# Optimization experiments

Hardware: AMD Instinct MI355X
Metric: run time of the kernel (lower is better)

The kernel has to match this reference:

```python
import jax, jax.numpy as jnp
import numpy as np

H = 16          # num_attention_heads
HD = 64         # hidden_size_per_attention_head
EPS = 1e-12

def _layernorm(x, w, b):
    u = x.mean(-1, keepdims=True)
    s = ((x - u) ** 2).mean(-1, keepdims=True)
    return w * (x - u) / jnp.sqrt(s + EPS) + b

def _split_heads(x):
    b, s, d = x.shape
    return x.reshape(b, s, H, d // H).transpose(0, 2, 1, 3)  # [b,h,s,hd]

def _merge_heads(x):
    b, h, s, hd = x.shape
    return x.transpose(0, 2, 1, 3).reshape(b, s, h * hd)


def setup_inputs() -> dict:
    key = jax.random.key(0)
    ks = jax.random.split(key, 20)
    B, S, T, D, F = 4, 1024, 1024, 1024, 4096
    w = lambda k, shp: (jax.random.normal(k, shp, jnp.float32) * 0.02)
    return {
        "hidden_states": jax.random.normal(ks[0], (B, S, D), jnp.float32),
        "enc_hidden_states": jax.random.normal(ks[1], (B, T, D), jnp.float32),
        "enc_attn_mask": jnp.zeros((B, 1, 1, T), jnp.float32),
        "dec_attn_mask": jnp.tril(jnp.ones((S, S), jnp.float32)).reshape(1, 1, S, S),
        "ln1_w": jnp.ones((D,), jnp.float32), "ln1_b": jnp.zeros((D,), jnp.float32),
        "qkv_w": w(ks[2], (D, 3 * D)), "qkv_b": jnp.zeros((3 * D,), jnp.float32),
        "attn_o_w": w(ks[3], (D, D)), "attn_o_b": jnp.zeros((D,), jnp.float32),
        "ln2_w": jnp.ones((D,), jnp.float32), "ln2_b": jnp.zeros((D,), jnp.float32),
        "q_w": w(ks[4], (D, D)), "q_b": jnp.zeros((D,), jnp.float32),
        "kv_w": w(ks[5], (D, 2 * D)), "kv_b": jnp.zeros((2 * D,), jnp.float32),
        "ca_o_w": w(ks[6], (D, D)), "ca_o_b": jnp.zeros((D,), jnp.float32),
        "ln3_w": jnp.ones((D,), jnp.float32), "ln3_b": jnp.zeros((D,), jnp.float32),
        "ffn_in_w": w(ks[7], (D, F)), "ffn_in_b": jnp.zeros((F,), jnp.float32),
        "ffn_out_w": w(ks[8], (F, D)), "ffn_out_b": jnp.zeros((D,), jnp.float32),
    }


def reference(hidden_states, enc_hidden_states, enc_attn_mask, dec_attn_mask,
              ln1_w, ln1_b, qkv_w, qkv_b, attn_o_w, attn_o_b,
              ln2_w, ln2_b, q_w, q_b, kv_w, kv_b, ca_o_w, ca_o_b,
              ln3_w, ln3_b, ffn_in_w, ffn_in_b, ffn_out_w, ffn_out_b):
    scale = 1.0 / jnp.sqrt(jnp.float32(HD))
    # dropout layers are identity (eval mode)

    # ---- self-attention (ltor multiplicative mask formula) ----
    residual = hidden_states
    x = _layernorm(hidden_states, ln1_w, ln1_b)
    qkv = x @ qkv_w + qkv_b
    q, k, v = jnp.split(qkv, 3, axis=-1)
    q, k, v = _split_heads(q), _split_heads(k), _split_heads(v)
    scores = jnp.einsum('bhsd,bhtd->bhst', q, k) * scale
    scores = scores * dec_attn_mask - 10000.0 * (1.0 - dec_attn_mask)
    probs = jax.nn.softmax(scores, axis=-1)
    ctx = _merge_heads(jnp.einsum('bhst,bhtd->bhsd', probs, v))
    hidden_states = residual + (ctx @ attn_o_w + attn_o_b)

    # ---- cross-attention (additive enc mask) ----
    residual = hidden_states
    x = _layernorm(hidden_states, ln2_w, ln2_b)
    q = _split_heads(x @ q_w + q_b)
    kv = enc_hidden_states @ kv_w + kv_b
    k, v = jnp.split(kv, 2, axis=-1)
    k, v = _split_heads(k), _split_heads(v)
    scores = jnp.einsum('bhsd,bhtd->bhst', q, k) * scale + enc_attn_mask
    probs = jax.nn.softmax(scores, axis=-1)
    ctx = _merge_heads(jnp.einsum('bhst,bhtd->bhsd', probs, v))
    hidden_states = residual + (ctx @ ca_o_w + ca_o_b)

    # ---- FFN ----
    residual = hidden_states
    x = _layernorm(hidden_states, ln3_w, ln3_b)
    x = jax.nn.gelu(x @ ffn_in_w + ffn_in_b, approximate=False)
    x = x @ ffn_out_w + ffn_out_b
    return residual + x
```

## Files before the change

### kernel.cpp

```cpp
#include <hip/hip_runtime.h>
#include <cstdint>
#include <cstddef>

typedef unsigned short u16;
typedef __bf16 bf16x8 __attribute__((ext_vector_type(8)));
typedef float f32x4 __attribute__((ext_vector_type(4)));

__device__ __forceinline__ u16 f2bf(float f) {
  unsigned u = __float_as_uint(f);
  u += 0x7fffu + ((u >> 16) & 1u);
  return (u16)(u >> 16);
}

__device__ __forceinline__ float block_sum(float v, float* sbuf, int tid) {
#pragma unroll
  for (int off = 1; off < 64; off <<= 1) v += __shfl_xor(v, off, 64);
  if ((tid & 63) == 0) sbuf[tid >> 6] = v;
  __syncthreads();
  v = sbuf[0] + sbuf[1] + sbuf[2] + sbuf[3];
  __syncthreads();
  return v;
}

__device__ __forceinline__ void gld16(const void* g, void* l) {
  __builtin_amdgcn_global_load_lds((const __attribute__((address_space(1))) void*)g,
                                   (__attribute__((address_space(3))) void*)l,
                                   16, 0, 0);
}



#define BIG_PREAMBLE(BM, Kdim, KB)                                               \
  constexpr int NQA = (BM) / 64;                                                 \
  constexpr int IF  = (BM) / 32;                                                 \
  const int tid = threadIdx.x;                                                   \
  const int lane = tid & 63, wave = tid >> 6;                                    \
  const int l15 = lane & 15, g = (lane >> 4) & 3;                                \
  const int wr = (wave >> 2) * ((BM) / 2), wc = (wave & 3) * 64;                 \
  const int gx = gridDim.x;                                                      \
  const int nwg = gx * gridDim.y;                                                \
  const int id = blockIdx.y * gx + blockIdx.x;                                   \
  const int qq = nwg >> 3, rr = nwg & 7;                                         \
  const int xcd = id & 7, slot = id >> 3;                                        \
  const int sid = (xcd < rr ? xcd * (qq + 1) : rr * (qq + 1) + (xcd - rr) * qq) + slot; \
  const int bx = sid % gx, by = sid / gx;                                        \
  const int m0 = by * (BM), n0 = bx * 256;                                       \
  size_t aoff[NQA]; int adst[NQA];                                               \
  size_t boff[4];   int bdst[4];                                                 \
  _Pragma("unroll")                                                              \
  for (int q = 0; q < NQA; ++q) {                                                \
    const int c = tid + q * 512, row = c >> 3, ch = (c & 7) ^ (row & 7);         \
    aoff[q] = (size_t)(m0 + row) * (Kdim) + ch * 8 + (KB);                       \
    adst[q] = c * 8;                                                             \
  }                                                                              \
  _Pragma("unroll")                                                              \
  for (int q = 0; q < 4; ++q) {                                                  \
    const int c = tid + q * 512, row = c >> 3, ch = (c & 7) ^ (row & 7);         \
    boff[q] = (size_t)(n0 + row) * (Kdim) + ch * 8 + (KB);                       \
    bdst[q] = c * 8;                                                             \
  }

#define BIG_STAGE(BM, kk, buf)                                                   \
  {                                                                              \
    _Pragma("unroll")                                                            \
    for (int q = 0; q < NQA; ++q) gld16(A + aoff[q] + (kk), As + (buf) * ((BM) * 64) + adst[q]); \
    _Pragma("unroll")                                                            \
    for (int q = 0; q < 4; ++q)  gld16(B + boff[q] + (kk), Bs + (buf) * 16384 + bdst[q]); \
  }

#define BIG_COMPUTE(BM, buf)                                                     \
  {                                                                              \
    _Pragma("unroll")                                                            \
    for (int ks = 0; ks < 2; ++ks) {                                             \
      const int chR = (((ks * 4 + g) ^ (l15 & 7)) * 8);                          \
      bf16x8 af[IF], bg[4];                                                      \
      _Pragma("unroll")                                                          \
      for (int i = 0; i < IF; ++i)                                               \
        af[i] = *(const bf16x8*)(As + (buf) * ((BM) * 64) + (wr + i * 16 + l15) * 64 + chR); \
      _Pragma("unroll")                                                          \
      for (int j = 0; j < 4; ++j)                                                \
        bg[j] = *(const bf16x8*)(Bs + (buf) * 16384 + (wc + j * 16 + l15) * 64 + chR); \
      _Pragma("unroll")                                                          \
      for (int i = 0; i < IF; ++i)                                               \
        _Pragma("unroll")                                                        \
        for (int j = 0; j < 4; ++j)                                              \
          acc[i][j] = __builtin_amdgcn_mfma_f32_16x16x32_bf16(af[i], bg[j], acc[i][j], 0, 0, 0); \
    }                                                                            \
  }

#define BIG_WAIT_PREV(BM)                                                        \
  if constexpr ((BM) == 256)      asm volatile("s_waitcnt vmcnt(8)\ns_barrier" ::: "memory"); \
  else if constexpr ((BM) == 128) asm volatile("s_waitcnt vmcnt(6)\ns_barrier" ::: "memory"); \
  else                            asm volatile("s_waitcnt vmcnt(5)\ns_barrier" ::: "memory");

#define BIG_KLOOP(BM, NT)                                                        \
  f32x4 acc[IF][4] = {};                                                         \
  BIG_STAGE(BM, 0, 0)                                                            \
  int cur = 0;                                                                   \
  for (int t = 0; t < (NT) - 1; ++t) {                                           \
    BIG_STAGE(BM, (t + 1) * 64, cur ^ 1)                                         \
    BIG_WAIT_PREV(BM)                                                            \
    BIG_COMPUTE(BM, cur)                                                         \
    asm volatile("s_waitcnt lgkmcnt(0)\ns_barrier" ::: "memory");                \
    cur ^= 1;                                                                    \
  }                                                                              \
  asm volatile("s_waitcnt vmcnt(0)\ns_barrier" ::: "memory");                    \
  BIG_COMPUTE(BM, cur)

template<int BM, int MODE>
__global__ __launch_bounds__(512, 2) void gemm_big(
    const u16* __restrict__ A, const u16* __restrict__ B,
    const float* __restrict__ bias,
    u16* __restrict__ out0, u16* __restrict__ out1, u16* __restrict__ out2,
    int N, int K)
{
  __shared__ __align__(16) u16 As[2 * BM * 64];
  __shared__ __align__(16) u16 Bs[2 * 256 * 64];
  BIG_PREAMBLE(BM, K, 0)
  const int NT = K >> 6;
  BIG_KLOOP(BM, NT)

  if constexpr (MODE == 0) {
#pragma unroll
    for (int i = 0; i < IF; ++i) {
#pragma unroll
      for (int j = 0; j < 4; ++j) {
        const int col = n0 + wc + j * 16 + l15;
        const float bs = bias[col];
#pragma unroll
        for (int r = 0; r < 4; ++r) {
          const int gm = m0 + wr + i * 16 + g * 4 + r;
          float v = acc[i][j][r] + bs;
          v = 0.5f * v * (1.0f + erff(v * 0.70710678118654752f));
          out0[(size_t)gm * N + col] = f2bf(v);
        }
      }
    }
  } else {
#pragma unroll
    for (int i = 0; i < IF; ++i) {
#pragma unroll
      for (int j = 0; j < 4; ++j) {
        const int col = n0 + wc + j * 16 + l15;
        const int sec = (n0 + wc + j * 16) >> 10;
        const int tgt = (MODE == 1) ? sec : sec + 1;
        const float bs = bias[col];
#pragma unroll
        for (int r = 0; r < 4; ++r) {
          const int gm = m0 + wr + i * 16 + g * 4 + r;
          const float v = acc[i][j][r] + bs;
          const int cl = col & 1023, h = cl >> 6, d = cl & 63;
          const int z = (gm >> 10) * 16 + h, s = gm & 1023;
          if (tgt == 0)
            out0[((size_t)z * 1024 + s) * 64 + d] = f2bf(v * 0.125f);
          else if (tgt == 1)
            out1[((((size_t)z * 8 + (s >> 7)) * 8 + (d >> 3)) * 128 + (s & 127)) * 8 + (d & 7)] = f2bf(v);
          else
            out2[((size_t)z * 8 + (s >> 7)) * 8192 + (((s >> 3) & 15) * 64 + d) * 8 + (s & 7)] = f2bf(v);
        }
      }
    }
  }
}

template<int BM>
__global__ __launch_bounds__(512, 2) void gemm_part(
    const u16* __restrict__ A, const u16* __restrict__ B,
    float* __restrict__ part, int K, int Klen)
{
  __shared__ __align__(16) u16 As[2 * BM * 64];
  __shared__ __align__(16) u16 Bs[2 * 256 * 64];
  const int kb = blockIdx.z * Klen;
  float* outP = part + (size_t)blockIdx.z * (4096ULL * 1024);
  BIG_PREAMBLE(BM, K, kb)
  const int NT = Klen >> 6;
  BIG_KLOOP(BM, NT)

#pragma unroll
  for (int i = 0; i < IF; ++i)
#pragma unroll
    for (int j = 0; j < 4; ++j) {
      const int col = n0 + wc + j * 16 + l15;
#pragma unroll
      for (int r = 0; r < 4; ++r) {
        const int gm = m0 + wr + i * 16 + g * 4 + r;
        outP[(size_t)gm * 1024 + col] = acc[i][j][r];
      }
    }
}

__global__ __launch_bounds__(256, 2) void flash_attn(
    const u16* __restrict__ qh, const u16* __restrict__ kt, const u16* __restrict__ vt,
    const float* __restrict__ emask, u16* __restrict__ ctx, int causal)
{
  __shared__ __align__(16) u16 sK[8192];
  __shared__ __align__(16) u16 sV[8192];
  __shared__ __align__(16) u16 sP[128 * 72];

  const int tid = threadIdx.x, lane = tid & 63, wave = tid >> 6;
  const int l15 = lane & 15, g = (lane >> 4) & 3;
  const int id = blockIdx.y * 8 + blockIdx.x;
  const int xcd = id & 7, slot = id >> 3;
  const int z = xcd * 8 + (slot >> 3), b = z >> 4, h = z & 15;
  const int m0 = (slot & 7) * 128;
  const int r0 = wave * 32;

  bf16x8 qf[2][2];
  {
    const u16* qz = qh + ((size_t)z * 1024 + m0 + r0 + l15) * 64 + g * 8;
#pragma unroll
    for (int i2 = 0; i2 < 2; ++i2)
#pragma unroll
      for (int kc = 0; kc < 2; ++kc)
        qf[i2][kc] = *(const bf16x8*)(qz + (size_t)i2 * 16 * 64 + kc * 32);
  }

  float m_i[2][4], l_i[2][4];
#pragma unroll
  for (int i2 = 0; i2 < 2; ++i2)
#pragma unroll
    for (int r = 0; r < 4; ++r) { m_i[i2][r] = -1.0e30f; l_i[i2][r] = 0.0f; }

  f32x4 o[2][4] = {};
  const int tmax = causal ? m0 : 896;

  for (int t0 = 0; t0 <= tmax; t0 += 128) {
    const u16* ktile = kt + ((size_t)z * 8 + (t0 >> 7)) * 8192;
    const u16* vtile = vt + ((size_t)z * 8 + (t0 >> 7)) * 8192;
    __syncthreads();
#pragma unroll
    for (int i = 0; i < 4; ++i) {
      const int off = (wave * 4 + i) * 512 + lane * 8;
      gld16(ktile + off, sK + off);
      gld16(vtile + off, sV + off);
    }
    __syncthreads();

#pragma unroll
    for (int ci = 0; ci < 2; ++ci) {
      if (causal && t0 == m0 && ci * 64 > r0 + 31) continue;

      f32x4 sa[2][4] = {};
#pragma unroll
      for (int kc = 0; kc < 2; ++kc) {
        bf16x8 bg[4];
#pragma unroll
        for (int jn = 0; jn < 4; ++jn)
          bg[jn] = *(const bf16x8*)(sK + ((kc * 4 + g) * 128 + ci * 64 + jn * 16 + l15) * 8);
#pragma unroll
        for (int i2 = 0; i2 < 2; ++i2)
#pragma unroll
          for (int jn = 0; jn < 4; ++jn)
            sa[i2][jn] = __builtin_amdgcn_mfma_f32_16x16x32_bf16(qf[i2][kc], bg[jn], sa[i2][jn], 0, 0, 0);
      }

      if (causal) {
        if (t0 == m0 && ci * 64 + 63 > r0) {
#pragma unroll
          for (int i2 = 0; i2 < 2; ++i2)
#pragma unroll
            for (int jn = 0; jn < 4; ++jn) {
              const int col = ci * 64 + jn * 16 + l15;
#pragma unroll
              for (int r = 0; r < 4; ++r) {
                const int row = r0 + i2 * 16 + g * 4 + r;
                if (col > row) sa[i2][jn][r] = -3.0e38f;
              }
            }
        }
      } else {
#pragma unroll
        for (int jn = 0; jn < 4; ++jn) {
          const float mv = emask[(size_t)b * 1024 + t0 + ci * 64 + jn * 16 + l15];
#pragma unroll
          for (int i2 = 0; i2 < 2; ++i2)
#pragma unroll
            for (int r = 0; r < 4; ++r) sa[i2][jn][r] += mv;
        }
      }

      float alpha[2][4];
#pragma unroll
      for (int i2 = 0; i2 < 2; ++i2)
#pragma unroll
        for (int r = 0; r < 4; ++r) {
          const int rowl = r0 + i2 * 16 + g * 4 + r;
          float v = fmaxf(fmaxf(sa[i2][0][r], sa[i2][1][r]), fmaxf(sa[i2][2][r], sa[i2][3][r]));
          v = fmaxf(v, __shfl_xor(v, 1, 64));
          v = fmaxf(v, __shfl_xor(v, 2, 64));
          v = fmaxf(v, __shfl_xor(v, 4, 64));
          v = fmaxf(v, __shfl_xor(v, 8, 64));
          const float mo = m_i[i2][r];
          const float mn = fmaxf(mo, v);
          m_i[i2][r] = mn;
          alpha[i2][r] = __expf(mo - mn);
          float s = 0.0f;
#pragma unroll
          for (int jn = 0; jn < 4; ++jn) {
            const float p = __expf(sa[i2][jn][r] - mn);
            s += p;
            sP[rowl * 72 + jn * 16 + l15] = f2bf(p);
          }
          s += __shfl_xor(s, 1, 64);
          s += __shfl_xor(s, 2, 64);
          s += __shfl_xor(s, 4, 64);
          s += __shfl_xor(s, 8, 64);
          l_i[i2][r] = alpha[i2][r] * l_i[i2][r] + s;
        }

#pragma unroll
      for (int i2 = 0; i2 < 2; ++i2)
#pragma unroll
        for (int jn = 0; jn < 4; ++jn)
#pragma unroll
          for (int r = 0; r < 4; ++r)
            o[i2][jn][r] *= alpha[i2][r];

      asm volatile("s_waitcnt lgkmcnt(0)" ::: "memory");
#pragma unroll
      for (int kc2 = 0; kc2 < 2; ++kc2) {
        bf16x8 pa[2], vb[4];
#pragma unroll
        for (int i2 = 0; i2 < 2; ++i2)
          pa[i2] = *(const bf16x8*)(sP + (r0 + i2 * 16 + l15) * 72 + kc2 * 32 + g * 8);
#pragma unroll
        for (int jn = 0; jn < 4; ++jn)
          vb[jn] = *(const bf16x8*)(sV + ((ci * 8 + kc2 * 4 + g) * 64 + jn * 16 + l15) * 8);
#pragma unroll
        for (int i2 = 0; i2 < 2; ++i2)
#pragma unroll
          for (int jn = 0; jn < 4; ++jn)
            o[i2][jn] = __builtin_amdgcn_mfma_f32_16x16x32_bf16(pa[i2], vb[jn], o[i2][jn], 0, 0, 0);
      }
    }
  }

#pragma unroll
  for (int i2 = 0; i2 < 2; ++i2)
#pragma unroll
    for (int r = 0; r < 4; ++r) {
      const float inv = 1.0f / l_i[i2][r];
      const size_t base = ((size_t)(b * 1024 + m0 + r0 + i2 * 16 + g * 4 + r)) * 1024 + h * 64;
#pragma unroll
      for (int jn = 0; jn < 4; ++jn)
        ctx[base + jn * 16 + l15] = f2bf(o[i2][jn][r] * inv);
    }
}

struct PrepArgs {
  const float* w[7]; u16* wt[7]; int K[7]; int N[7]; int cum[7];
  const float* enc; u16* enc_bf;
  const float* hid; const float* ln1w; const float* ln1b; u16* xln;
};
__global__ __launch_bounds__(256) void prep_kernel(PrepArgs a) {
  __shared__ float t[32][33];
  __shared__ float sbuf[4];
  const int bb = blockIdx.x, tid = threadIdx.x;
  if (bb < 16384) {
    int wi = 0;
#pragma unroll
    for (int i = 0; i < 7; ++i) if (bb >= a.cum[i]) wi = i + 1; else break;
    const int base = wi ? a.cum[wi - 1] : 0;
    const int tileIdx = bb - base;
    const int Kd = a.K[wi], Nd = a.N[wi], nx = Nd >> 5;
    const int n0 = (tileIdx % nx) * 32, k0 = (tileIdx / nx) * 32;
    const float* w = a.w[wi]; u16* wt = a.wt[wi];
    const int tx = tid & 31, ty = tid >> 5;
#pragma unroll
    for (int r = ty; r < 32; r += 8) t[r][tx] = w[(size_t)(k0 + r) * Nd + n0 + tx];
    __syncthreads();
#pragma unroll
    for (int r = ty; r < 32; r += 8) wt[(size_t)(n0 + r) * Kd + k0 + tx] = f2bf(t[tx][r]);
  } else if (bb < 20480) {
    const size_t i = ((size_t)(bb - 16384) * 256 + tid) * 4;
    const float4 v = *(const float4*)(a.enc + i);
    ushort4 o; o.x = f2bf(v.x); o.y = f2bf(v.y); o.z = f2bf(v.z); o.w = f2bf(v.w);
    *(ushort4*)(a.enc_bf + i) = o;
  } else {
    const int row = bb - 20480;
    const float4 v = *(const float4*)(a.hid + (size_t)row * 1024 + tid * 4);
    float s = block_sum(v.x + v.y + v.z + v.w, sbuf, tid);
    const float u = s * (1.0f / 1024.0f);
    const float d0 = v.x - u, d1 = v.y - u, d2 = v.z - u, d3 = v.w - u;
    float sq = block_sum(d0 * d0 + d1 * d1 + d2 * d2 + d3 * d3, sbuf, tid);
    const float rstd = rsqrtf(sq * (1.0f / 1024.0f) + 1e-12f);
    const int c = tid * 4;
    ushort4 o;
    o.x = f2bf(a.ln1w[c + 0] * d0 * rstd + a.ln1b[c + 0]);
    o.y = f2bf(a.ln1w[c + 1] * d1 * rstd + a.ln1b[c + 1]);
    o.z = f2bf(a.ln1w[c + 2] * d2 * rstd + a.ln1b[c + 2]);
    o.w = f2bf(a.ln1w[c + 3] * d3 * rstd + a.ln1b[c + 3]);
    *(ushort4*)(a.xln + (size_t)row * 1024 + c) = o;
  }
}

__global__ __launch_bounds__(256) void ln_red1_kernel(
    const float* __restrict__ p0,
    const float* __restrict__ bias, const float* __restrict__ res,
    const float* __restrict__ w, const float* __restrict__ b,
    float* __restrict__ hOut, u16* __restrict__ xln)
{
  __shared__ float sbuf[4];
  const int row = blockIdx.x, tid = threadIdx.x;
  const size_t off = (size_t)row * 1024 + tid * 4;
  const int c = tid * 4;
  const float4 a0 = *(const float4*)(p0 + off);
  const float4 bs = *(const float4*)(bias + c);
  const float4 rs = *(const float4*)(res + off);
  float4 v;
  v.x = a0.x + bs.x + rs.x;
  v.y = a0.y + bs.y + rs.y;
  v.z = a0.z + bs.z + rs.z;
  v.w = a0.w + bs.w + rs.w;
  *(float4*)(hOut + off) = v;
  float s = block_sum(v.x + v.y + v.z + v.w, sbuf, tid);
  const float u = s * (1.0f / 1024.0f);
  const float d0 = v.x - u, d1 = v.y - u, d2 = v.z - u, d3 = v.w - u;
  float sq = block_sum(d0 * d0 + d1 * d1 + d2 * d2 + d3 * d3, sbuf, tid);
  const float rstd = rsqrtf(sq * (1.0f / 1024.0f) + 1e-12f);
  ushort4 o;
  o.x = f2bf(w[c + 0] * d0 * rstd + b[c + 0]);
  o.y = f2bf(w[c + 1] * d1 * rstd + b[c + 1]);
  o.z = f2bf(w[c + 2] * d2 * rstd + b[c + 2]);
  o.w = f2bf(w[c + 3] * d3 * rstd + b[c + 3]);
  *(ushort4*)(xln + off) = o;
}

__global__ __launch_bounds__(256) void reduce_q1_kernel(
    const float* __restrict__ p0,
    const float* __restrict__ bias, u16* __restrict__ qh)
{
  const int m = blockIdx.x, tid = threadIdx.x;
  const size_t off = (size_t)m * 1024 + tid * 4;
  const int n = tid * 4, h = n >> 6, d = n & 63;
  const int b = m >> 10, s = m & 1023;
  const float4 a0 = *(const float4*)(p0 + off);
  const float4 bs = *(const float4*)(bias + n);
  ushort4 o;
  o.x = f2bf((a0.x + bs.x) * 0.125f);
  o.y = f2bf((a0.y + bs.y) * 0.125f);
  o.z = f2bf((a0.z + bs.z) * 0.125f);
  o.w = f2bf((a0.w + bs.w) * 0.125f);
  *(ushort4*)(qh + ((size_t)((b * 16 + h) * 1024 + s)) * 64 + d) = o;
}

__global__ __launch_bounds__(256) void reduce_out_kernel(
    const float* __restrict__ p0, const float* __restrict__ p1,
    const float* __restrict__ bias, const float* __restrict__ res,
    float* __restrict__ out)
{
  const int m = blockIdx.x, tid = threadIdx.x;
  const size_t off = (size_t)m * 1024 + tid * 4;
  const int c = tid * 4;
  const float4 a0 = *(const float4*)(p0 + off);
  const float4 a1 = *(const float4*)(p1 + off);
  const float4 bs = *(const float4*)(bias + c);
  const float4 rs = *(const float4*)(res + off);
  float4 v;
  v.x = a0.x + a1.x + bs.x + rs.x;
  v.y = a0.y + a1.y + bs.y + rs.y;
  v.z = a0.z + a1.z + bs.z + rs.z;
  v.w = a0.w + a1.w + bs.w + rs.w;
  *(float4*)(out + off) = v;
}

constexpr size_t MB = 1024ULL * 1024;
constexpr size_t WT_QKV    = 0;
constexpr size_t WT_ATTN_O = 6 * MB;
constexpr size_t WT_Q      = 8 * MB;
constexpr size_t WT_KV     = 10 * MB;
constexpr size_t WT_CA_O   = 14 * MB;
constexpr size_t WT_FFN_IN = 16 * MB;
constexpr size_t WT_FFN_OUT= 24 * MB;
constexpr size_t ENC_BF    = 32 * MB;
constexpr size_t XLN       = 40 * MB;
constexpr size_t QH        = 48 * MB;
constexpr size_t KT        = 56 * MB;
constexpr size_t VT        = 64 * MB;
constexpr size_t CTX       = 72 * MB;
constexpr size_t HBUF      = 80 * MB;
constexpr size_t SP0       = 96 * MB;
constexpr size_t SP1       = 112 * MB;
constexpr size_t FFN_MID   = 128 * MB;

extern "C" void kernel_launch(void* const* d_in, const int* in_sizes, int n_in,
                              void* d_out, int out_size, void* d_ws, size_t ws_size,
                              hipStream_t stream) {
  const float* hidden   = (const float*)d_in[0];
  const float* enc      = (const float*)d_in[1];
  const float* encm     = (const float*)d_in[2];
  const float* ln1w = (const float*)d_in[4],  *ln1b = (const float*)d_in[5];
  const float* qkv_w = (const float*)d_in[6], *qkv_b = (const float*)d_in[7];
  const float* attn_o_w = (const float*)d_in[8], *attn_o_b = (const float*)d_in[9];
  const float* ln2w = (const float*)d_in[10], *ln2b = (const float*)d_in[11];
  const float* q_w = (const float*)d_in[12],  *q_b = (const float*)d_in[13];
  const float* kv_w = (const float*)d_in[14], *kv_b = (const float*)d_in[15];
  const float* ca_o_w = (const float*)d_in[16], *ca_o_b = (const float*)d_in[17];
  const float* ln3w = (const float*)d_in[18], *ln3b = (const float*)d_in[19];
  const float* ffn_in_w = (const float*)d_in[20], *ffn_in_b = (const float*)d_in[21];
  const float* ffn_out_w = (const float*)d_in[22], *ffn_out_b = (const float*)d_in[23];

  char* ws = (char*)d_ws;
  u16* wt_qkv    = (u16*)(ws + WT_QKV);
  u16* wt_attn_o = (u16*)(ws + WT_ATTN_O);
  u16* wt_q      = (u16*)(ws + WT_Q);
  u16* wt_kv     = (u16*)(ws + WT_KV);
  u16* wt_ca_o   = (u16*)(ws + WT_CA_O);
  u16* wt_ffn_in = (u16*)(ws + WT_FFN_IN);
  u16* wt_ffn_out= (u16*)(ws + WT_FFN_OUT);
  u16* enc_bf = (u16*)(ws + ENC_BF);
  u16* xln    = (u16*)(ws + XLN);
  u16* qh     = (u16*)(ws + QH);
  u16* kt     = (u16*)(ws + KT);
  u16* vt     = (u16*)(ws + VT);
  u16* ctx    = (u16*)(ws + CTX);
  float* hF   = (float*)(ws + HBUF);
  float* sp0  = (float*)(ws + SP0);
  float* sp1  = (float*)(ws + SP1);
  u16* ffn_mid = (u16*)(ws + FFN_MID);

  PrepArgs pa;
  pa.w[0] = qkv_w;    pa.wt[0] = wt_qkv;     pa.K[0] = 1024; pa.N[0] = 3072; pa.cum[0] = 3072;
  pa.w[1] = attn_o_w; pa.wt[1] = wt_attn_o;  pa.K[1] = 1024; pa.N[1] = 1024; pa.cum[1] = 4096;
  pa.w[2] = q_w;      pa.wt[2] = wt_q;       pa.K[2] = 1024; pa.N[2] = 1024; pa.cum[2] = 5120;
  pa.w[3] = kv_w;     pa.wt[3] = wt_kv;      pa.K[3] = 1024; pa.N[3] = 2048; pa.cum[3] = 7168;
  pa.w[4] = ca_o_w;   pa.wt[4] = wt_ca_o;    pa.K[4] = 1024; pa.N[4] = 1024; pa.cum[4] = 8192;
  pa.w[5] = ffn_in_w; pa.wt[5] = wt_ffn_in;  pa.K[5] = 1024; pa.N[5] = 4096; pa.cum[5] = 12288;
  pa.w[6] = ffn_out_w;pa.wt[6] = wt_ffn_out; pa.K[6] = 4096; pa.N[6] = 1024; pa.cum[6] = 16384;
  pa.enc = enc; pa.enc_bf = enc_bf;
  pa.hid = hidden; pa.ln1w = ln1w; pa.ln1b = ln1b; pa.xln = xln;
  prep_kernel<<<24576, 256, 0, stream>>>(pa);

  gemm_big<256, 1><<<dim3(12, 16), 512, 0, stream>>>(xln, wt_qkv, qkv_b, qh, kt, vt, 3072, 1024);
  flash_attn<<<dim3(8, 64), 256, 0, stream>>>(qh, kt, vt, nullptr, ctx, 1);
  gemm_part<64><<<dim3(4, 64, 1), 512, 0, stream>>>(ctx, wt_attn_o, sp0, 1024, 1024);
  ln_red1_kernel<<<4096, 256, 0, stream>>>(sp0, attn_o_b, hidden, ln2w, ln2b, hF, xln);

  gemm_part<64><<<dim3(4, 64, 1), 512, 0, stream>>>(xln, wt_q, sp0, 1024, 1024);
  reduce_q1_kernel<<<4096, 256, 0, stream>>>(sp0, q_b, qh);
  gemm_big<128, 3><<<dim3(8, 32), 512, 0, stream>>>(enc_bf, wt_kv, kv_b, nullptr, kt, vt, 2048, 1024);
  flash_attn<<<dim3(8, 64), 256, 0, stream>>>(qh, kt, vt, encm, ctx, 0);
  gemm_part<64><<<dim3(4, 64, 1), 512, 0, stream>>>(ctx, wt_ca_o, sp0, 1024, 1024);
  ln_red1_kernel<<<4096, 256, 0, stream>>>(sp0, ca_o_b, hF, ln3w, ln3b, hF, xln);

  gemm_big<256, 0><<<dim3(16, 16), 512, 0, stream>>>(xln, wt_ffn_in, ffn_in_b, ffn_mid, nullptr, nullptr, 4096, 1024);
  gemm_part<128><<<dim3(4, 32, 2), 512, 0, stream>>>(ffn_mid, wt_ffn_out, sp0, 4096, 2048);
  reduce_out_kernel<<<4096, 256, 0, stream>>>(sp0, sp1, ffn_out_b, hF, (float*)d_out);
}
```

Before: 555.4 us.

## Shrink flash-attention query tile to 64 rows and swizzle P buffer

The flash attention kernel now processes 64 query rows per block (16 per wave) instead of 128, doubling the grid and raising the occupancy hint from 2 to 4 blocks per SM. The P staging buffer becomes a compact 64x64 tile with an XOR swizzle in place of row padding, to avoid LDS bank conflicts. More, smaller blocks should balance the causal triangle better and hide latency, but each K/V tile is now loaded from global memory twice as often.

Result: no change. 558.2 us (+0.5%).

```diff
diff --git a/kernel.cpp b/kernel.cpp
--- a/kernel.cpp
+++ b/kernel.cpp
@@ -189,40 +189,38 @@
     }
 }
 
-__global__ __launch_bounds__(256, 2) void flash_attn(
+__global__ __launch_bounds__(256, 4) void flash_attn(
     const u16* __restrict__ qh, const u16* __restrict__ kt, const u16* __restrict__ vt,
     const float* __restrict__ emask, u16* __restrict__ ctx, int causal)
 {
   __shared__ __align__(16) u16 sK[8192];
   __shared__ __align__(16) u16 sV[8192];
-  __shared__ __align__(16) u16 sP[128 * 72];
+  __shared__ __align__(16) u16 sP[64 * 64];
 
   const int tid = threadIdx.x, lane = tid & 63, wave = tid >> 6;
   const int l15 = lane & 15, g = (lane >> 4) & 3;
   const int id = blockIdx.y * 8 + blockIdx.x;
   const int xcd = id & 7, slot = id >> 3;
-  const int z = xcd * 8 + (slot >> 3), b = z >> 4, h = z & 15;
-  const int m0 = (slot & 7) * 128;
-  const int r0 = wave * 32;
-
-  bf16x8 qf[2][2];
+  const int z = xcd * 8 + (slot >> 4), b = z >> 4, h = z & 15;
+  const int q0 = (slot & 15) * 64;
+  const int r0 = wave * 16;
+  const int qrel = q0 & 64;
+
+  bf16x8 qf[2];
   {
-    const u16* qz = qh + ((size_t)z * 1024 + m0 + r0 + l15) * 64 + g * 8;
-#pragma unroll
-    for (int i2 = 0; i2 < 2; ++i2)
-#pragma unroll
-      for (int kc = 0; kc < 2; ++kc)
-        qf[i2][kc] = *(const bf16x8*)(qz + (size_t)i2 * 16 * 64 + kc * 32);
-  }
-
-  float m_i[2][4], l_i[2][4];
-#pragma unroll
-  for (int i2 = 0; i2 < 2; ++i2)
-#pragma unroll
-    for (int r = 0; r < 4; ++r) { m_i[i2][r] = -1.0e30f; l_i[i2][r] = 0.0f; }
-
-  f32x4 o[2][4] = {};
-  const int tmax = causal ? m0 : 896;
+    const u16* qz = qh + ((size_t)z * 1024 + q0 + r0 + l15) * 64 + g * 8;
+#pragma unroll
+    for (int kc = 0; kc < 2; ++kc)
+      qf[kc] = *(const bf16x8*)(qz + kc * 32);
+  }
+
+  float m_i[4], l_i[4];
+#pragma unroll
+  for (int r = 0; r < 4; ++r) { m_i[r] = -1.0e30f; l_i[r] = 0.0f; }
+
+  f32x4 o[4] = {};
+  const int dt = (q0 >> 7) << 7;
+  const int tmax = causal ? dt : 896;
 
   for (int t0 = 0; t0 <= tmax; t0 += 128) {
     const u16* ktile = kt + ((size_t)z * 8 + (t0 >> 7)) * 8192;
@@ -238,9 +236,9 @@
 
 #pragma unroll
     for (int ci = 0; ci < 2; ++ci) {
-      if (causal && t0 == m0 && ci * 64 > r0 + 31) continue;
-
-      f32x4 sa[2][4] = {};
+      if (causal && t0 == dt && ci * 64 > qrel + r0 + 15) continue;
+
+      f32x4 sa[4] = {};
 #pragma unroll
       for (int kc = 0; kc < 2; ++kc) {
         bf16x8 bg[4];
@@ -248,103 +246,88 @@
         for (int jn = 0; jn < 4; ++jn)
           bg[jn] = *(const bf16x8*)(sK + ((kc * 4 + g) * 128 + ci * 64 + jn * 16 + l15) * 8);
 #pragma unroll
-        for (int i2 = 0; i2 < 2; ++i2)
-#pragma unroll
-          for (int jn = 0; jn < 4; ++jn)
-            sa[i2][jn] = __builtin_amdgcn_mfma_f32_16x16x32_bf16(qf[i2][kc], bg[jn], sa[i2][jn], 0, 0, 0);
+        for (int jn = 0; jn < 4; ++jn)
+          sa[jn] = __builtin_amdgcn_mfma_f32_16x16x32_bf16(qf[kc], bg[jn], sa[jn], 0, 0, 0);
       }
 
       if (causal) {
-        if (t0 == m0 && ci * 64 + 63 > r0) {
-#pragma unroll
-          for (int i2 = 0; i2 < 2; ++i2)
-#pragma unroll
-            for (int jn = 0; jn < 4; ++jn) {
-              const int col = ci * 64 + jn * 16 + l15;
-#pragma unroll
-              for (int r = 0; r < 4; ++r) {
-                const int row = r0 + i2 * 16 + g * 4 + r;
-                if (col > row) sa[i2][jn][r] = -3.0e38f;
-              }
+        if (t0 == dt && ci * 64 + 63 > qrel + r0) {
+#pragma unroll
+          for (int jn = 0; jn < 4; ++jn) {
+            const int col = ci * 64 + jn * 16 + l15;
+#pragma unroll
+            for (int r = 0; r < 4; ++r) {
+              const int row = qrel + r0 + g * 4 + r;
+              if (col > row) sa[jn][r] = -3.0e38f;
             }
+          }
         }
       } else {
 #pragma unroll
         for (int jn = 0; jn < 4; ++jn) {
           const float mv = emask[(size_t)b * 1024 + t0 + ci * 64 + jn * 16 + l15];
 #pragma unroll
-          for (int i2 = 0; i2 < 2; ++i2)
-#pragma unroll
-            for (int r = 0; r < 4; ++r) sa[i2][jn][r] += mv;
+          for (int r = 0; r < 4; ++r) sa[jn][r] += mv;
         }
       }
 
-      float alpha[2][4];
-#pragma unroll
-      for (int i2 = 0; i2 < 2; ++i2)
-#pragma unroll
-        for (int r = 0; r < 4; ++r) {
-          const int rowl = r0 + i2 * 16 + g * 4 + r;
-          float v = fmaxf(fmaxf(sa[i2][0][r], sa[i2][1][r]), fmaxf(sa[i2][2][r], sa[i2][3][r]));
-          v = fmaxf(v, __shfl_xor(v, 1, 64));
-          v = fmaxf(v, __shfl_xor(v, 2, 64));
-          v = fmaxf(v, __shfl_xor(v, 4, 64));
-          v = fmaxf(v, __shfl_xor(v, 8, 64));
-          const float mo = m_i[i2][r];
-          const float mn = fmaxf(mo, v);
-          m_i[i2][r] = mn;
-          alpha[i2][r] = __expf(mo - mn);
-          float s = 0.0f;
-#pragma unroll
-          for (int jn = 0; jn < 4; ++jn) {
-            const float p = __expf(sa[i2][jn][r] - mn);
-            s += p;
-            sP[rowl * 72 + jn * 16 + l15] = f2bf(p);
-          }
-          s += __shfl_xor(s, 1, 64);
-          s += __shfl_xor(s, 2, 64);
-          s += __shfl_xor(s, 4, 64);
-          s += __shfl_xor(s, 8, 64);
-          l_i[i2][r] = alpha[i2][r] * l_i[i2][r] + s;
+      float alpha[4];
+#pragma unroll
+      for (int r = 0; r < 4; ++r) {
+        const int rowl = r0 + g * 4 + r;
+        const int swzr = (rowl & 7) << 4;
+        float v = fmaxf(fmaxf(sa[0][r], sa[1][r]), fmaxf(sa[2][r], sa[3][r]));
+        v = fmaxf(v, __shfl_xor(v, 1, 64));
+        v = fmaxf(v, __shfl_xor(v, 2, 64));
+        v = fmaxf(v, __shfl_xor(v, 4, 64));
+        v = fmaxf(v, __shfl_xor(v, 8, 64));
+        const float mo = m_i[r];
+        const float mn = fmaxf(mo, v);
+        m_i[r] = mn;
+        alpha[r] = __expf(mo - mn);
+        float s = 0.0f;
+#pragma unroll
+        for (int jn = 0; jn < 4; ++jn) {
+          const float p = __expf(sa[jn][r] - mn);
+          s += p;
+          sP[(rowl * 128 + ((jn * 32 + 2 * l15) ^ swzr)) >> 1] = f2bf(p);
         }
-
-#pragma unroll
-      for (int i2 = 0; i2 < 2; ++i2)
-#pragma unroll
-        for (int jn = 0; jn < 4; ++jn)
-#pragma unroll
-          for (int r = 0; r < 4; ++r)
-            o[i2][jn][r] *= alpha[i2][r];
+        s += __shfl_xor(s, 1, 64);
+        s += __shfl_xor(s, 2, 64);
+        s += __shfl_xor(s, 4, 64);
+        s += __shfl_xor(s, 8, 64);
+        l_i[r] = alpha[r] * l_i[r] + s;
+      }
+
+#pragma unroll
+      for (int jn = 0; jn < 4; ++jn)
+#pragma unroll
+        for (int r = 0; r < 4; ++r)
+          o[jn][r] *= alpha[r];
 
       asm volatile("s_waitcnt lgkmcnt(0)" ::: "memory");
 #pragma unroll
       for (int kc2 = 0; kc2 < 2; ++kc2) {
-        bf16x8 pa[2], vb[4];
-#pragma unroll
-        for (int i2 = 0; i2 < 2; ++i2)
-          pa[i2] = *(const bf16x8*)(sP + (r0 + i2 * 16 + l15) * 72 + kc2 * 32 + g * 8);
+        bf16x8 pa, vb[4];
+        pa = *(const bf16x8*)(sP + (((r0 + l15) * 128 + ((kc2 * 64 + g * 16) ^ ((l15 & 7) << 4))) >> 1));
 #pragma unroll
         for (int jn = 0; jn < 4; ++jn)
           vb[jn] = *(const bf16x8*)(sV + ((ci * 8 + kc2 * 4 + g) * 64 + jn * 16 + l15) * 8);
 #pragma unroll
-        for (int i2 = 0; i2 < 2; ++i2)
-#pragma unroll
-          for (int jn = 0; jn < 4; ++jn)
-            o[i2][jn] = __builtin_amdgcn_mfma_f32_16x16x32_bf16(pa[i2], vb[jn], o[i2][jn], 0, 0, 0);
+        for (int jn = 0; jn < 4; ++jn)
+          o[jn] = __builtin_amdgcn_mfma_f32_16x16x32_bf16(pa, vb[jn], o[jn], 0, 0, 0);
       }
     }
   }
 
 #pragma unroll
-  for (int i2 = 0; i2 < 2; ++i2)
-#pragma unroll
-    for (int r = 0; r < 4; ++r) {
-      const float inv = 1.0f / l_i[i2][r];
-      const size_t base = ((size_t)(b * 1024 + m0 + r0 + i2 * 16 + g * 4 + r)) * 1024 + h * 64;
-#pragma unroll
-      for (int jn = 0; jn < 4; ++jn)
-        ctx[base + jn * 16 + l15] = f2bf(o[i2][jn][r] * inv);
-    }
+  for (int r = 0; r < 4; ++r) {
+    const float inv = 1.0f / l_i[r];
+    const size_t base = ((size_t)(b * 1024 + q0 + r0 + g * 4 + r)) * 1024 + h * 64;
+#pragma unroll
+    for (int jn = 0; jn < 4; ++jn)
+      ctx[base + jn * 16 + l15] = f2bf(o[jn][r] * inv);
+  }
 }
 
 struct PrepArgs {
@@ -532,14 +515,14 @@
   prep_kernel<<<24576, 256, 0, stream>>>(pa);
 
   gemm_big<256, 1><<<dim3(12, 16), 512, 0, stream>>>(xln, wt_qkv, qkv_b, qh, kt, vt, 3072, 1024);
-  flash_attn<<<dim3(8, 64), 256, 0, stream>>>(qh, kt, vt, nullptr, ctx, 1);
+  flash_attn<<<dim3(8, 128), 256, 0, stream>>>(qh, kt, vt, nullptr, ctx, 1);
   gemm_part<64><<<dim3(4, 64, 1), 512, 0, stream>>>(ctx, wt_attn_o, sp0, 1024, 1024);
   ln_red1_kernel<<<4096, 256, 0, stream>>>(sp0, attn_o_b, hidden, ln2w, ln2b, hF, xln);
 
   gemm_part<64><<<dim3(4, 64, 1), 512, 0, stream>>>(xln, wt_q, sp0, 1024, 1024);
   reduce_q1_kernel<<<4096, 256, 0, stream>>>(sp0, q_b, qh);
   gemm_big<128, 3><<<dim3(8, 32), 512, 0, stream>>>(enc_bf, wt_kv, kv_b, nullptr, kt, vt, 2048, 1024);
-  flash_attn<<<dim3(8, 64), 256, 0, stream>>>(qh, kt, vt, encm, ctx, 0);
+  flash_attn<<<dim3(8, 128), 256, 0, stream>>>(qh, kt, vt, encm, ctx, 0);
   gemm_part<64><<<dim3(4, 64, 1), 512, 0, stream>>>(ctx, wt_ca_o, sp0, 1024, 1024);
   ln_red1_kernel<<<4096, 256, 0, stream>>>(sp0, ca_o_b, hF, ln3w, ln3b, hF, xln);
 
```
